# Performance work log

Hardware: AMD Instinct MI355X
Metric: run time of the kernel (lower is better)

Reference implementation:

```python
import jax, jax.numpy as jnp
import numpy as np

IMAGE_SIZE = 224
BLUR_SIGMA = 4.0  # PIL ImageFilter.GaussianBlur(radius=4): radius acts as std dev
BLUR_RADIUS = 8   # truncate kernel at 2*sigma


def _gaussian_blur(x, sigma=BLUR_SIGMA, radius=BLUR_RADIUS):
    # separable gaussian blur on NCHW, SAME padding
    t = jnp.arange(-radius, radius + 1, dtype=x.dtype)
    kern = jnp.exp(-0.5 * (t / sigma) ** 2)
    kern = kern / kern.sum()
    dn = ('NCHW', 'OIHW', 'NCHW')
    x = jax.lax.conv_general_dilated(x, kern.reshape(1, 1, 1, -1), (1, 1), 'SAME', dimension_numbers=dn)
    x = jax.lax.conv_general_dilated(x, kern.reshape(1, 1, -1, 1), (1, 1), 'SAME', dimension_numbers=dn)
    return x


def setup_inputs() -> dict:
    key = jax.random.key(0)
    ks = jax.random.split(key, 8)
    N = 1000
    inp = {
        'z': jax.random.normal(ks[0], (1, 512), jnp.float32),
        'fmap0': jax.random.normal(ks[1], (1, 64, 56, 56), jnp.float32),
        'fmap1': jax.random.normal(ks[2], (1, 128, 28, 28), jnp.float32),
        'fmap2': jax.random.normal(ks[3], (1, 256, 14, 14), jnp.float32),
        'z_lib': jax.random.normal(ks[4], (N, 512), jnp.float32),
        'lib0': jax.random.normal(ks[5], (N, 64, 56, 56), jnp.float32),
        'lib1': jax.random.normal(ks[6], (N, 128, 28, 28), jnp.float32),
        'lib2': jax.random.normal(ks[7], (N, 256, 14, 14), jnp.float32),
        'k': 5,
    }
    return inp


def reference(z, fmap0, fmap1, fmap2, z_lib, lib0, lib1, lib2, k):
    # distances = ||z_lib - z||_2 over feature dim -> [N]
    dists = jnp.linalg.norm(z_lib - z, axis=1)
    # topk smallest
    neg_vals, indices = jax.lax.top_k(-dists, k)
    z_score = (-neg_vals).mean()

    s_total = jnp.zeros((1, 1, IMAGE_SIZE, IMAGE_SIZE), jnp.float32)
    for fmap, lib in ((fmap0, lib0), (fmap1, lib1), (fmap2, lib2)):
        nearest = lib[indices]                            # [k, C, H, W]
        s = jnp.linalg.norm(nearest - fmap, axis=1)        # [k, H, W] (channel-wise L2)
        s = s.min(axis=0, keepdims=True)                   # [1, H, W]
        s_up = jax.image.resize(s[None], (1, 1, IMAGE_SIZE, IMAGE_SIZE), method='bilinear')
        s_total = s_total + s_up
    s_total = _gaussian_blur(s_total)
    return z_score, s_total
```

## Files before the change

### kernel.cpp

```cpp
#include <hip/hip_runtime.h>
#include <hip/hip_bf16.h>
#include <math.h>

#define IMG 224
#define NLIB 1000
#define ZD 512
#define MAXK 8
#define NTHR 512
#define KA_BLK 125
#define KB_BLK 196
#define S0F (2 * MAXK * 3136)
#define S1F (4 * MAXK * 784)
#define S2F (8 * MAXK * 196)
#define SFLOATS (S0F + S1F + S2F)

__device__ __forceinline__ int clampk(int k) {
    if (k < 1) k = 1;
    if (k > MAXK) k = MAXK;
    return k;
}

__device__ __forceinline__ void cgs_f32(float* p, float v) {
    __hip_atomic_store(p, v, __ATOMIC_RELAXED, __HIP_MEMORY_SCOPE_AGENT);
}
__device__ __forceinline__ float cgl_f32(const float* p) {
    return __hip_atomic_load((float*)p, __ATOMIC_RELAXED, __HIP_MEMORY_SCOPE_AGENT);
}

__global__ void __launch_bounds__(NTHR) k_pre(const float* __restrict__ z,
                                              const float* __restrict__ zlib,
                                              float* __restrict__ dists,
                                              float* __restrict__ sfill) {
    int tid = threadIdx.x, lane = tid & 63, wave = tid >> 6, bid = blockIdx.x;

    for (int g = bid * NTHR + tid; g < SFLOATS; g += KA_BLK * NTHR)
        cgs_f32(sfill + g, -1.0f);

    int gw = bid * 8 + wave;
    const float4* row4 = (const float4*)(zlib + (size_t)gw * ZD);
    const float4* z4   = (const float4*)z;
    float4 a0 = row4[lane],      b0 = z4[lane];
    float4 a1 = row4[64 + lane], b1 = z4[64 + lane];
    float acc = 0.f, d;
    d = a0.x - b0.x; acc += d * d;  d = a0.y - b0.y; acc += d * d;
    d = a0.z - b0.z; acc += d * d;  d = a0.w - b0.w; acc += d * d;
    d = a1.x - b1.x; acc += d * d;  d = a1.y - b1.y; acc += d * d;
    d = a1.z - b1.z; acc += d * d;  d = a1.w - b1.w; acc += d * d;
#pragma unroll
    for (int off = 32; off > 0; off >>= 1) acc += __shfl_xor(acc, off, 64);
    if (lane == 0) dists[gw] = sqrtf(acc);
}

template<int K, int P>
__device__ float poll_min(const float* base, int strideK, int strideP, int pix) {
    float v[K][P];
    long guard = 0;
    for (;;) {
        bool ok = true;
#pragma unroll
        for (int kq = 0; kq < K; ++kq)
#pragma unroll
            for (int pp = 0; pp < P; ++pp)
                v[kq][pp] = cgl_f32(base + (size_t)pp * strideP + kq * strideK + pix);
#pragma unroll
        for (int kq = 0; kq < K; ++kq)
#pragma unroll
            for (int pp = 0; pp < P; ++pp)
                ok &= (v[kq][pp] >= 0.f);
        if (ok) break;
        if (++guard > 20000000L) break;
        __builtin_amdgcn_s_sleep(1);
    }
    float m = 3.4e38f;
#pragma unroll
    for (int kq = 0; kq < K; ++kq) {
        float s = 0.f;
#pragma unroll
        for (int pp = 0; pp < P; ++pp) s += v[kq][pp];
        m = fminf(m, s);
    }
    return m;
}

template<int P>
__device__ __forceinline__ float poll_min_k(int k, const float* base, int sK, int sP, int pix) {
    switch (k) {
        case 1: return poll_min<1, P>(base, sK, sP, pix);
        case 2: return poll_min<2, P>(base, sK, sP, pix);
        case 3: return poll_min<3, P>(base, sK, sP, pix);
        case 4: return poll_min<4, P>(base, sK, sP, pix);
        case 5: return poll_min<5, P>(base, sK, sP, pix);
        case 6: return poll_min<6, P>(base, sK, sP, pix);
        case 7: return poll_min<7, P>(base, sK, sP, pix);
        default: return poll_min<8, P>(base, sK, sP, pix);
    }
}

__device__ __forceinline__ float bilin(const float* __restrict__ msm, int Wl, int Win,
                                       int bx, int by, float scl, int gx, int gy) {
    float sxf = ((float)gx + 0.5f) * scl - 0.5f;
    float syf = ((float)gy + 0.5f) * scl - 0.5f;
    float fx = floorf(sxf), fy = floorf(syf);
    float wx = sxf - fx,    wy = syf - fy;
    int ix = (int)fx, iy = (int)fy;
    int x0c = min(max(ix, 0), Win - 1) - bx, x1c = min(max(ix + 1, 0), Win - 1) - bx;
    int y0c = min(max(iy, 0), Win - 1) - by, y1c = min(max(iy + 1, 0), Win - 1) - by;
    float v00 = msm[y0c * Wl + x0c], v10 = msm[y0c * Wl + x1c];
    float v01 = msm[y1c * Wl + x0c], v11 = msm[y1c * Wl + x1c];
    return (1.f - wy) * ((1.f - wx) * v00 + wx * v10) +
           wy * ((1.f - wx) * v01 + wx * v11);
}

__global__ void __launch_bounds__(NTHR) k_main(
        const float* __restrict__ f0, const float* __restrict__ f1,
        const float* __restrict__ f2,
        const float* __restrict__ l0, const float* __restrict__ l1,
        const float* __restrict__ l2,
        const float* __restrict__ dists, const int* __restrict__ kp,
        float* __restrict__ out,
        float* __restrict__ s0, float* __restrict__ s1, float* __restrict__ s2) {

    __shared__ float msm0[100], msm1[36], msm2[9];
    __shared__ float pre[32 * 32];
    __shared__ float mid[32 * 16];
    __shared__ float wk[17];

    int tid = threadIdx.x, lane = tid & 63, wv = tid >> 6, bid = blockIdx.x;
    int k = clampk(*kp);

    if (tid < 17) {
        float r = (float)(tid - 8) * 0.25f;
        wk[tid] = expf(-0.5f * r * r);
    }

    int tx = bid % 14, ty = bid / 14;
    int x0 = tx * 16, y0 = ty * 16;
    int b0x = x0 / 4 - 3,  b0y = y0 / 4 - 3;
    int b1x = x0 / 8 - 2,  b1y = y0 / 8 - 2;
    int b2x = x0 / 16 - 1, b2y = y0 / 16 - 1;

    int n0 = k * 1568, n1 = k * 784, n2 = k * 392;
    int njobs = n0 + n1 + n2;
    int nwj = (njobs + 63) >> 6;
    if (wv < 2) {
        int s = bid + KB_BLK * wv;
        bool havejob = (s < nwj);
        bool scorer = (bid == 0 && wv == 0);
        if (havejob || scorer) {
            float vals[16];
#pragma unroll
            for (int q = 0; q < 16; ++q) {
                int e = lane + 64 * q;
                vals[q] = (e < NLIB) ? dists[e] : 3.4e38f;
            }
            int idxr[8];
            float ssum = 0.f;
#pragma unroll
            for (int it = 0; it < 8; ++it) {
                if (it < k) {
                    float bv = 3.4e38f; int bi = 0x7fffffff;
#pragma unroll
                    for (int q = 0; q < 16; ++q) {
                        if (vals[q] < bv) { bv = vals[q]; bi = lane + 64 * q; }
                    }
#pragma unroll
                    for (int off = 1; off < 64; off <<= 1) {
                        float ov = __shfl_xor(bv, off, 64);
                        int   oi = __shfl_xor(bi, off, 64);
                        if (ov < bv || (ov == bv && oi < bi)) { bv = ov; bi = oi; }
                    }
#pragma unroll
                    for (int q = 0; q < 16; ++q) {
                        if (lane + 64 * q == bi) vals[q] = 3.4e38f;
                    }
                    idxr[it] = bi; ssum += bv;
                } else idxr[it] = 0;
            }
            if (scorer && lane == 0) out[0] = ssum / (float)k;

            if (havejob) {
                int j = s * 64 + lane;
                if (j < njobs) {
                    const float* fmp; const float* lbp; float* op;
                    int kk, pq, cbase, HW, Cfull;
                    if (j < n0) {
                        int r = j;           kk = r / 1568; int q = r % 1568;
                        int part = q / 784;  pq = q % 784;  cbase = part * 32;
                        HW = 3136; Cfull = 64;  fmp = f0; lbp = l0;
                        op = s0 + part * (MAXK * 3136) + kk * 3136;
                    } else if (j < n0 + n1) {
                        int r = j - n0;      kk = r / 784;  int q = r % 784;
                        int part = q / 196;  pq = q % 196;  cbase = part * 32;
                        HW = 784;  Cfull = 128; fmp = f1; lbp = l1;
                        op = s1 + part * (MAXK * 784) + kk * 784;
                    } else {
                        int r = j - n0 - n1; kk = r / 392;  int q = r % 392;
                        int part = q / 49;   pq = q % 49;   cbase = part * 32;
                        HW = 196;  Cfull = 256; fmp = f2; lbp = l2;
                        op = s2 + part * (MAXK * 196) + kk * 196;
                    }
                    int myidx = 0;
#pragma unroll
                    for (int it = 0; it < 8; ++it) if (it == kk) myidx = idxr[it];

                    const float4* lb4 = (const float4*)(lbp + (size_t)myidx * (size_t)Cfull * HW
                                                            + (size_t)cbase * HW);
                    const float4* fb4 = (const float4*)(fmp + (size_t)cbase * HW);
                    int HW4 = HW >> 2;
                    float ax = 0.f, ay = 0.f, az = 0.f, aw = 0.f;
#pragma unroll
                    for (int c = 0; c < 32; ++c) {
                        float4 a = lb4[c * HW4 + pq];
                        float4 b = fb4[c * HW4 + pq];
                        float dx = a.x - b.x, dy = a.y - b.y, dz = a.z - b.z, dw = a.w - b.w;
                        ax += dx * dx; ay += dy * dy; az += dz * dz; aw += dw * dw;
                    }
                    float* o = op + 4 * pq;
                    cgs_f32(o + 0, ax); cgs_f32(o + 1, ay);
                    cgs_f32(o + 2, az); cgs_f32(o + 3, aw);
                }
            }
        }
    }

    if (tid >= 128 && tid < 128 + 145) {
        int i = tid - 128;
        float m;
        if (i < 100) {
            int ly = i / 10, lx = i % 10;
            int gx = min(max(b0x + lx, 0), 55), gy = min(max(b0y + ly, 0), 55);
            m = poll_min_k<2>(k, s0, 3136, MAXK * 3136, gy * 56 + gx);
            msm0[i] = sqrtf(m);
        } else if (i < 136) {
            int r = i - 100; int ly = r / 6, lx = r % 6;
            int gx = min(max(b1x + lx, 0), 27), gy = min(max(b1y + ly, 0), 27);
            m = poll_min_k<4>(k, s1, 784, MAXK * 784, gy * 28 + gx);
            msm1[r] = sqrtf(m);
        } else {
            int r = i - 136; int ly = r / 3, lx = r % 3;
            int gx = min(max(b2x + lx, 0), 13), gy = min(max(b2y + ly, 0), 13);
            m = poll_min_k<8>(k, s2, 196, MAXK * 196, gy * 14 + gx);
            msm2[r] = sqrtf(m);
        }
    }
    __syncthreads();

    float wsum = 0.f;
#pragma unroll
    for (int t = 0; t < 17; ++t) wsum += wk[t];
    float inv2 = 1.f / (wsum * wsum);

    for (int i = tid; i < 32 * 32; i += NTHR) {
        int lx = i % 32, ly = i / 32;
        int gx = x0 - 8 + lx, gy = y0 - 8 + ly;
        float v = 0.f;
        if ((unsigned)gx < (unsigned)IMG && (unsigned)gy < (unsigned)IMG) {
            v = bilin(msm0, 10, 56, b0x, b0y, 0.25f,   gx, gy)
              + bilin(msm1, 6,  28, b1x, b1y, 0.125f,  gx, gy)
              + bilin(msm2, 3,  14, b2x, b2y, 0.0625f, gx, gy);
        }
        pre[i] = v;
    }
    __syncthreads();

    if (tid < 32 * 16) {
        int cx = tid % 16, ly = tid / 16;
        float acc = 0.f;
#pragma unroll
        for (int t = 0; t < 17; ++t) acc += wk[t] * pre[ly * 32 + cx + t];
        mid[ly * 16 + cx] = acc;
    }
    __syncthreads();

    if (tid < 16 * 16) {
        int ox = tid % 16, oy = tid / 16;
        float acc = 0.f;
#pragma unroll
        for (int t = 0; t < 17; ++t) acc += wk[t] * mid[(oy + t) * 16 + ox];
        out[1 + (y0 + oy) * IMG + (x0 + ox)] = acc * inv2;
    }
}

extern "C" void kernel_launch(void* const* d_in, const int* in_sizes, int n_in,
                              void* d_out, int out_size, void* d_ws, size_t ws_size,
                              hipStream_t stream) {
    const float* z    = (const float*)d_in[0];
    const float* f0   = (const float*)d_in[1];
    const float* f1   = (const float*)d_in[2];
    const float* f2   = (const float*)d_in[3];
    const float* zlib = (const float*)d_in[4];
    const float* l0   = (const float*)d_in[5];
    const float* l1   = (const float*)d_in[6];
    const float* l2   = (const float*)d_in[7];
    const int*   kp   = (const int*)d_in[8];
    float* out = (float*)d_out;

    float* ws    = (float*)d_ws;
    float* dists = ws;
    float* s0    = ws + 1024;
    float* s1    = s0 + S0F;
    float* s2    = s1 + S1F;

    k_pre<<<KA_BLK, NTHR, 0, stream>>>(z, zlib, dists, s0);
    k_main<<<KB_BLK, NTHR, 0, stream>>>(f0, f1, f2, l0, l1, l2, dists, kp, out,
                                        s0, s1, s2);
}
```

Baseline: 26.22 us.

## Compute top-k once in k_pre via inter-block flag barrier

Before, every job wave in k_main redid the top-k selection over 1000 distances on its own. Now block 0 of k_pre waits on per-block completion flags, computes top-k and the z-score once, and writes the indices to workspace. k_main then simply reads idxs[kk]. This removes redundant shuffle-heavy selection from many waves, but it adds a spin-wait grid barrier at the tail of k_pre. That barrier depends on all 125 blocks being co-resident, and the serial top-k now sits on the critical path before k_main starts.

```diff
diff --git a/kernel.cpp b/kernel.cpp
--- a/kernel.cpp
+++ b/kernel.cpp
@@ -9,6 +9,7 @@
 #define NTHR 512
 #define KA_BLK 125
 #define KB_BLK 196
+#define MTAG 0x5EEDF00Du
 #define S0F (2 * MAXK * 3136)
 #define S1F (4 * MAXK * 784)
 #define S2F (8 * MAXK * 196)
@@ -20,6 +21,12 @@
     return k;
 }
 
+__device__ __forceinline__ void cgs_u32(unsigned* p, unsigned v) {
+    __hip_atomic_store(p, v, __ATOMIC_RELAXED, __HIP_MEMORY_SCOPE_AGENT);
+}
+__device__ __forceinline__ unsigned cgl_u32(unsigned* p) {
+    return __hip_atomic_load(p, __ATOMIC_RELAXED, __HIP_MEMORY_SCOPE_AGENT);
+}
 __device__ __forceinline__ void cgs_f32(float* p, float v) {
     __hip_atomic_store(p, v, __ATOMIC_RELAXED, __HIP_MEMORY_SCOPE_AGENT);
 }
@@ -27,28 +34,85 @@
     return __hip_atomic_load((float*)p, __ATOMIC_RELAXED, __HIP_MEMORY_SCOPE_AGENT);
 }
 
-__global__ void __launch_bounds__(NTHR) k_pre(const float* __restrict__ z,
-                                              const float* __restrict__ zlib,
-                                              float* __restrict__ dists,
-                                              float* __restrict__ sfill) {
+__global__ void __launch_bounds__(NTHR) k_pre(
+        const float* __restrict__ z, const float* __restrict__ zlib,
+        const int* __restrict__ kp,
+        float* __restrict__ dists, unsigned* __restrict__ d1,
+        int* __restrict__ idxs, float* __restrict__ out,
+        float* __restrict__ sfill) {
     int tid = threadIdx.x, lane = tid & 63, wave = tid >> 6, bid = blockIdx.x;
+    int k = clampk(*kp);
 
     for (int g = bid * NTHR + tid; g < SFLOATS; g += KA_BLK * NTHR)
         cgs_f32(sfill + g, -1.0f);
 
     int gw = bid * 8 + wave;
-    const float4* row4 = (const float4*)(zlib + (size_t)gw * ZD);
-    const float4* z4   = (const float4*)z;
-    float4 a0 = row4[lane],      b0 = z4[lane];
-    float4 a1 = row4[64 + lane], b1 = z4[64 + lane];
-    float acc = 0.f, d;
-    d = a0.x - b0.x; acc += d * d;  d = a0.y - b0.y; acc += d * d;
-    d = a0.z - b0.z; acc += d * d;  d = a0.w - b0.w; acc += d * d;
-    d = a1.x - b1.x; acc += d * d;  d = a1.y - b1.y; acc += d * d;
-    d = a1.z - b1.z; acc += d * d;  d = a1.w - b1.w; acc += d * d;
-#pragma unroll
-    for (int off = 32; off > 0; off >>= 1) acc += __shfl_xor(acc, off, 64);
-    if (lane == 0) dists[gw] = sqrtf(acc);
+    {
+        const float4* row4 = (const float4*)(zlib + (size_t)gw * ZD);
+        const float4* z4   = (const float4*)z;
+        float4 a0 = row4[lane],      b0 = z4[lane];
+        float4 a1 = row4[64 + lane], b1 = z4[64 + lane];
+        float acc = 0.f, d;
+        d = a0.x - b0.x; acc += d * d;  d = a0.y - b0.y; acc += d * d;
+        d = a0.z - b0.z; acc += d * d;  d = a0.w - b0.w; acc += d * d;
+        d = a1.x - b1.x; acc += d * d;  d = a1.y - b1.y; acc += d * d;
+        d = a1.z - b1.z; acc += d * d;  d = a1.w - b1.w; acc += d * d;
+#pragma unroll
+        for (int off = 32; off > 0; off >>= 1) acc += __shfl_xor(acc, off, 64);
+        if (lane == 0) cgs_f32(&dists[gw], sqrtf(acc));
+    }
+    __syncthreads();
+    if (tid == 0) cgs_u32(d1 + bid, MTAG);
+    if (bid != 0 || wave != 0) return;
+
+    {
+        unsigned pend = 0;
+#pragma unroll
+        for (int q = 0; q < 2; ++q) { int i = q * 64 + lane; if (i < KA_BLK) pend |= 1u << q; }
+        long guard = 0;
+        for (;;) {
+#pragma unroll
+            for (int q = 0; q < 2; ++q) {
+                int i = q * 64 + lane;
+                if ((pend & (1u << q)) && cgl_u32(d1 + i) == MTAG) pend &= ~(1u << q);
+            }
+            if (__all(pend == 0)) break;
+            if (++guard > 100000000L) break;
+            __builtin_amdgcn_s_sleep(2);
+        }
+    }
+    asm volatile("" ::: "memory");
+
+    float vals[16];
+#pragma unroll
+    for (int q = 0; q < 16; ++q) {
+        int e = lane + 64 * q;
+        vals[q] = (e < NLIB) ? cgl_f32(&dists[e]) : 3.4e38f;
+    }
+    float ssum = 0.f;
+    for (int it = 0; it < k; ++it) {
+        float bv = 3.4e38f; int bi = 0x7fffffff;
+#pragma unroll
+        for (int q = 0; q < 16; ++q) {
+            if (vals[q] < bv) { bv = vals[q]; bi = lane + 64 * q; }
+        }
+#pragma unroll
+        for (int off = 1; off < 64; off <<= 1) {
+            float ov = __shfl_xor(bv, off, 64);
+            int   oi = __shfl_xor(bi, off, 64);
+            if (ov < bv || (ov == bv && oi < bi)) { bv = ov; bi = oi; }
+        }
+#pragma unroll
+        for (int q = 0; q < 16; ++q) {
+            if (lane + 64 * q == bi) vals[q] = 3.4e38f;
+        }
+        if (lane == 0) idxs[it] = bi;
+        ssum += bv;
+    }
+    if (lane == 0) out[0] = ssum / (float)k;
+
+#pragma unroll
+    for (int q = 0; q < 2; ++q) { int i = q * 64 + lane; if (i < KA_BLK) cgs_u32(d1 + i, 0u); }
 }
 
 template<int K, int P>
@@ -116,7 +180,7 @@
         const float* __restrict__ f2,
         const float* __restrict__ l0, const float* __restrict__ l1,
         const float* __restrict__ l2,
-        const float* __restrict__ dists, const int* __restrict__ kp,
+        const int* __restrict__ idxs, const int* __restrict__ kp,
         float* __restrict__ out,
         float* __restrict__ s0, float* __restrict__ s1, float* __restrict__ s2) {
 
@@ -144,81 +208,43 @@
     int nwj = (njobs + 63) >> 6;
     if (wv < 2) {
         int s = bid + KB_BLK * wv;
-        bool havejob = (s < nwj);
-        bool scorer = (bid == 0 && wv == 0);
-        if (havejob || scorer) {
-            float vals[16];
-#pragma unroll
-            for (int q = 0; q < 16; ++q) {
-                int e = lane + 64 * q;
-                vals[q] = (e < NLIB) ? dists[e] : 3.4e38f;
-            }
-            int idxr[8];
-            float ssum = 0.f;
-#pragma unroll
-            for (int it = 0; it < 8; ++it) {
-                if (it < k) {
-                    float bv = 3.4e38f; int bi = 0x7fffffff;
-#pragma unroll
-                    for (int q = 0; q < 16; ++q) {
-                        if (vals[q] < bv) { bv = vals[q]; bi = lane + 64 * q; }
-                    }
-#pragma unroll
-                    for (int off = 1; off < 64; off <<= 1) {
-                        float ov = __shfl_xor(bv, off, 64);
-                        int   oi = __shfl_xor(bi, off, 64);
-                        if (ov < bv || (ov == bv && oi < bi)) { bv = ov; bi = oi; }
-                    }
-#pragma unroll
-                    for (int q = 0; q < 16; ++q) {
-                        if (lane + 64 * q == bi) vals[q] = 3.4e38f;
-                    }
-                    idxr[it] = bi; ssum += bv;
-                } else idxr[it] = 0;
-            }
-            if (scorer && lane == 0) out[0] = ssum / (float)k;
-
-            if (havejob) {
-                int j = s * 64 + lane;
-                if (j < njobs) {
-                    const float* fmp; const float* lbp; float* op;
-                    int kk, pq, cbase, HW, Cfull;
-                    if (j < n0) {
-                        int r = j;           kk = r / 1568; int q = r % 1568;
-                        int part = q / 784;  pq = q % 784;  cbase = part * 32;
-                        HW = 3136; Cfull = 64;  fmp = f0; lbp = l0;
-                        op = s0 + part * (MAXK * 3136) + kk * 3136;
-                    } else if (j < n0 + n1) {
-                        int r = j - n0;      kk = r / 784;  int q = r % 784;
-                        int part = q / 196;  pq = q % 196;  cbase = part * 32;
-                        HW = 784;  Cfull = 128; fmp = f1; lbp = l1;
-                        op = s1 + part * (MAXK * 784) + kk * 784;
-                    } else {
-                        int r = j - n0 - n1; kk = r / 392;  int q = r % 392;
-                        int part = q / 49;   pq = q % 49;   cbase = part * 32;
-                        HW = 196;  Cfull = 256; fmp = f2; lbp = l2;
-                        op = s2 + part * (MAXK * 196) + kk * 196;
-                    }
-                    int myidx = 0;
-#pragma unroll
-                    for (int it = 0; it < 8; ++it) if (it == kk) myidx = idxr[it];
-
-                    const float4* lb4 = (const float4*)(lbp + (size_t)myidx * (size_t)Cfull * HW
-                                                            + (size_t)cbase * HW);
-                    const float4* fb4 = (const float4*)(fmp + (size_t)cbase * HW);
-                    int HW4 = HW >> 2;
-                    float ax = 0.f, ay = 0.f, az = 0.f, aw = 0.f;
-#pragma unroll
-                    for (int c = 0; c < 32; ++c) {
-                        float4 a = lb4[c * HW4 + pq];
-                        float4 b = fb4[c * HW4 + pq];
-                        float dx = a.x - b.x, dy = a.y - b.y, dz = a.z - b.z, dw = a.w - b.w;
-                        ax += dx * dx; ay += dy * dy; az += dz * dz; aw += dw * dw;
-                    }
-                    float* o = op + 4 * pq;
-                    cgs_f32(o + 0, ax); cgs_f32(o + 1, ay);
-                    cgs_f32(o + 2, az); cgs_f32(o + 3, aw);
+        if (s < nwj) {
+            int j = s * 64 + lane;
+            if (j < njobs) {
+                const float* fmp; const float* lbp; float* op;
+                int kk, pq, cbase, HW, Cfull;
+                if (j < n0) {
+                    int r = j;           kk = r / 1568; int q = r % 1568;
+                    int part = q / 784;  pq = q % 784;  cbase = part * 32;
+                    HW = 3136; Cfull = 64;  fmp = f0; lbp = l0;
+                    op = s0 + part * (MAXK * 3136) + kk * 3136;
+                } else if (j < n0 + n1) {
+                    int r = j - n0;      kk = r / 784;  int q = r % 784;
+                    int part = q / 196;  pq = q % 196;  cbase = part * 32;
+                    HW = 784;  Cfull = 128; fmp = f1; lbp = l1;
+                    op = s1 + part * (MAXK * 784) + kk * 784;
+                } else {
+                    int r = j - n0 - n1; kk = r / 392;  int q = r % 392;
+                    int part = q / 49;   pq = q % 49;   cbase = part * 32;
+                    HW = 196;  Cfull = 256; fmp = f2; lbp = l2;
+                    op = s2 + part * (MAXK * 196) + kk * 196;
                 }
+                int myidx = idxs[kk];
+                const float4* lb4 = (const float4*)(lbp + (size_t)myidx * (size_t)Cfull * HW
+                                                        + (size_t)cbase * HW);
+                const float4* fb4 = (const float4*)(fmp + (size_t)cbase * HW);
+                int HW4 = HW >> 2;
+                float ax = 0.f, ay = 0.f, az = 0.f, aw = 0.f;
+#pragma unroll
+                for (int c = 0; c < 32; ++c) {
+                    float4 a = lb4[c * HW4 + pq];
+                    float4 b = fb4[c * HW4 + pq];
+                    float dx = a.x - b.x, dy = a.y - b.y, dz = a.z - b.z, dw = a.w - b.w;
+                    ax += dx * dx; ay += dy * dy; az += dz * dz; aw += dw * dw;
+                }
+                float* o = op + 4 * pq;
+                cgs_f32(o + 0, ax); cgs_f32(o + 1, ay);
+                cgs_f32(o + 2, az); cgs_f32(o + 3, aw);
             }
         }
     }
@@ -295,13 +321,15 @@
     const int*   kp   = (const int*)d_in[8];
     float* out = (float*)d_out;
 
-    float* ws    = (float*)d_ws;
-    float* dists = ws;
-    float* s0    = ws + 1024;
-    float* s1    = s0 + S0F;
-    float* s2    = s1 + S1F;
-
-    k_pre<<<KA_BLK, NTHR, 0, stream>>>(z, zlib, dists, s0);
-    k_main<<<KB_BLK, NTHR, 0, stream>>>(f0, f1, f2, l0, l1, l2, dists, kp, out,
+    float*    ws    = (float*)d_ws;
+    float*    dists = ws;
+    unsigned* d1    = (unsigned*)(ws + 1000);
+    int*      idxs  = (int*)(ws + 1152);
+    float*    s0    = ws + 1664;
+    float*    s1    = s0 + S0F;
+    float*    s2    = s1 + S1F;
+
+    k_pre<<<KA_BLK, NTHR, 0, stream>>>(z, zlib, kp, dists, d1, idxs, out, s0);
+    k_main<<<KB_BLK, NTHR, 0, stream>>>(f0, f1, f2, l0, l1, l2, idxs, kp, out,
                                         s0, s1, s2);
 }
```

New measurement: 24.13 us. 1.09x faster.
